# Kernel tuning notes

Measured on AMD Instinct MI355X. Metric: run time of the kernel, lower is better.

## Reference

```python
import jax, jax.numpy as jnp
import numpy as np
import math

EPS = 1e-5

def setup_inputs() -> dict:
    key = jax.random.key(0)
    ks = jax.random.split(key, 8)
    B, S, H, HD = 2, 4096, 2048, 128
    hidden_states = jax.random.normal(ks[0], (B, S, H), dtype=jnp.float32)
    attention_mask = jnp.zeros((1, S, S), dtype=jnp.float32)
    cos = jax.random.uniform(ks[1], (S, HD), dtype=jnp.float32)
    sin = jax.random.uniform(ks[2], (S, HD), dtype=jnp.float32)
    sc = 0.02
    wq = jax.random.normal(ks[3], (H, H), dtype=jnp.float32) * sc
    wk = jax.random.normal(ks[4], (H, H), dtype=jnp.float32) * sc
    wv = jax.random.normal(ks[5], (H, H), dtype=jnp.float32) * sc
    wo = jax.random.normal(ks[6], (H, H), dtype=jnp.float32) * sc
    return {"hidden_states": hidden_states, "attention_mask": attention_mask,
            "cos": cos, "sin": sin, "wq": wq, "wk": wk, "wv": wv, "wo": wo}


def _bitlinear(x, w):
    # BitNet 1.58b: ternarize weights (round(clamp(w/scale,-1,1))), dequant by mean|w|.
    scale = jnp.mean(jnp.abs(w))
    qw = jnp.round(jnp.clip(w / (scale + EPS), -1.0, 1.0))  # ternary {-1,0,1}
    dq = qw * scale
    return x @ dq.T


def _rotate_half(x):
    x1, x2 = jnp.split(x, 2, axis=-1)
    return jnp.concatenate((-x2, x1), axis=-1)


def _apply_rope(q, k, cos, sin):
    B, S, H = q.shape
    hd = cos.shape[-1]
    q4 = q.reshape(B, S, -1, hd)
    k4 = k.reshape(B, S, -1, hd)
    c = cos[None, :, None, :]  # [1,S,1,hd]
    s = sin[None, :, None, :]
    qe = q4 * c + _rotate_half(q4) * s
    ke = k4 * c + _rotate_half(k4) * s
    return qe.reshape(B, S, H), ke.reshape(B, S, H)


def reference(hidden_states, attention_mask, cos, sin, wq, wk, wv, wo):
    head_dim = cos.shape[-1]
    q = _bitlinear(hidden_states, wq)
    k = _bitlinear(hidden_states, wk)
    v = _bitlinear(hidden_states, wv)
    q, k = _apply_rope(q, k, cos, sin)
    # NOTE: original attends over the FULL hidden dim (no head split), scaled by sqrt(head_dim)
    scores = jnp.einsum('bqh,bkh->bqk', q, k) / math.sqrt(head_dim)
    scores = scores + attention_mask
    probs = jax.nn.softmax(scores, axis=-1)
    attn_out = jnp.einsum('bqk,bkh->bqh', probs, v)
    return _bitlinear(attn_out, wo)
```

## Files before the change

kernel.cpp:

```cpp
#include <hip/hip_runtime.h>
#include <hip/hip_bf16.h>
#include <stdint.h>

typedef _Float16 f16x8 __attribute__((ext_vector_type(8)));
typedef float f32x4 __attribute__((ext_vector_type(4)));
typedef unsigned short u16;

#define B_   2
#define S_   4096
#define H_   2048
#define M2_  8192
#define WELEMS (H_*H_)

__device__ __forceinline__ u16 f2h(float f) {
  _Float16 h = (_Float16)f;
  return __builtin_bit_cast(unsigned short, h);
}
__device__ __forceinline__ float h2f(u16 b) {
  _Float16 h = __builtin_bit_cast(_Float16, b);
  return (float)h;
}

__device__ __forceinline__ void gload16(const void* gptr, const void* lptr) {
  __builtin_amdgcn_global_load_lds(
      (const __attribute__((address_space(1))) void*)(uintptr_t)gptr,
      (__attribute__((address_space(3))) void*)(uint32_t)(uintptr_t)lptr,
      16, 0, 0);
}

template<int EPI>
__global__ __launch_bounds__(512, 2)
void gemm8(const u16* __restrict__ A, const u16* __restrict__ B,
           void* __restrict__ Cv, int K, int ldc, float cscale,
           long long sA, long long sB, long long sC)
{
  extern __shared__ char smem[];
  const int tid  = threadIdx.x;
  const int lane = tid & 63;
  const int wid  = tid >> 6;
  const int wm   = wid >> 2;
  const int wn   = wid & 3;

  const int gx  = gridDim.x;
  const int nwg = gx * gridDim.y;
  int f = blockIdx.y * gx + blockIdx.x;
  f = (f & 7) * (nwg >> 3) + (f >> 3);
  const int brow = (f / gx) << 8;
  const int bcol = (f % gx) << 8;
  const int z    = blockIdx.z;

  const u16* Ab = A + (size_t)z * sA;
  const u16* Bb = B + (size_t)z * sB;

  const int srow = ((tid >> 3) << 1) | ((tid >> 2) & 1);
  const int sk8  = (tid & 3) ^ ((tid >> 3) & 3);
  const u16* gA0 = Ab + (size_t)(brow + srow) * K + sk8 * 8;
  const u16* gA1 = gA0 + (size_t)128 * K;
  const u16* gB0 = Bb + (size_t)(bcol + srow) * K + sk8 * 8;
  const u16* gB1 = gB0 + (size_t)128 * K;

  char* ldsAw = smem + tid * 16;
  char* ldsBw = ldsAw + 65536;

  const int l15 = lane & 15;
  const int lanepart = ((l15 >> 1) << 7) |
                       ((((lane >> 4) ^ ((l15 >> 1) & 3))) << 4) |
                       ((lane & 1) << 6);
  const char* ldsA = smem + (wm << 13) + lanepart;
  const char* ldsB = smem + 65536 + (wn << 12) + lanepart;

  f32x4 acc[8][4];
  #pragma unroll
  for (int i = 0; i < 8; ++i)
    #pragma unroll
    for (int j = 0; j < 4; ++j) acc[i][j] = (f32x4){0.f, 0.f, 0.f, 0.f};

#define DS_A(BUF, MH, MR) (*(const f16x8*)(ldsA + (BUF)*16384 + (MH)*4096 + (MR)*1024))
#define DS_B(BUF, NR)     (*(const f16x8*)(ldsB + (BUF)*16384 + (NR)*1024))

#define MFMA4(AM, AV) \
  acc[AM][0] = __builtin_amdgcn_mfma_f32_16x16x32_f16(AV, b0, acc[AM][0], 0, 0, 0); \
  acc[AM][1] = __builtin_amdgcn_mfma_f32_16x16x32_f16(AV, b1, acc[AM][1], 0, 0, 0); \
  acc[AM][2] = __builtin_amdgcn_mfma_f32_16x16x32_f16(AV, b2, acc[AM][2], 0, 0, 0); \
  acc[AM][3] = __builtin_amdgcn_mfma_f32_16x16x32_f16(AV, b3, acc[AM][3], 0, 0, 0);

#define TILE(BUF, IBUF, DOISS, LASTT) do {                                    \
    if (LASTT) { asm volatile("s_waitcnt vmcnt(0)" ::: "memory"); }           \
    else       { asm volatile("s_waitcnt vmcnt(4)" ::: "memory"); }           \
    __builtin_amdgcn_s_barrier();                                             \
    if (DOISS) {                                                              \
      gload16(gA0, ldsAw + (IBUF)*16384);                                     \
      gload16(gA1, ldsAw + (IBUF)*16384 + 8192);                              \
    }                                                                         \
    f16x8 b0 = DS_B(BUF,0), b1 = DS_B(BUF,1), b2 = DS_B(BUF,2), b3 = DS_B(BUF,3); \
    f16x8 a0 = DS_A(BUF,0,0), a1 = DS_A(BUF,0,1), a2 = DS_A(BUF,0,2), a3 = DS_A(BUF,0,3); \
    asm volatile("s_waitcnt lgkmcnt(0)" ::: "memory");                        \
    __builtin_amdgcn_sched_barrier(0);                                        \
    __builtin_amdgcn_s_setprio(1);                                            \
    MFMA4(0, a0) MFMA4(1, a1) MFMA4(2, a2) MFMA4(3, a3)                       \
    __builtin_amdgcn_s_setprio(0);                                            \
    __builtin_amdgcn_s_barrier();                                             \
    if (DOISS) {                                                              \
      gload16(gB0, ldsBw + (IBUF)*16384);                                     \
      gload16(gB1, ldsBw + (IBUF)*16384 + 8192);                              \
      gA0 += 32; gA1 += 32; gB0 += 32; gB1 += 32;                             \
    }                                                                         \
    a0 = DS_A(BUF,1,0); a1 = DS_A(BUF,1,1); a2 = DS_A(BUF,1,2); a3 = DS_A(BUF,1,3); \
    asm volatile("s_waitcnt lgkmcnt(0)" ::: "memory");                        \
    __builtin_amdgcn_sched_barrier(0);                                        \
    __builtin_amdgcn_s_setprio(1);                                            \
    MFMA4(4, a0) MFMA4(5, a1) MFMA4(6, a2) MFMA4(7, a3)                       \
    __builtin_amdgcn_s_setprio(0);                                            \
  } while (0)

  gload16(gA0, ldsAw);          gload16(gA1, ldsAw + 8192);
  gload16(gB0, ldsBw);          gload16(gB1, ldsBw + 8192);
  gA0 += 32; gA1 += 32; gB0 += 32; gB1 += 32;
  gload16(gA0, ldsAw + 16384);  gload16(gA1, ldsAw + 16384 + 8192);
  gload16(gB0, ldsBw + 16384);  gload16(gB1, ldsBw + 16384 + 8192);
  gA0 += 32; gA1 += 32; gB0 += 32; gB1 += 32;

  const int NT4 = K >> 7;
  for (int it = 0; it < NT4; ++it) {
    const bool lst = (it == NT4 - 1);
    TILE(0, 2, true,  false);
    TILE(1, 3, true,  false);
    TILE(2, 0, !lst,  false);
    TILE(3, 1, !lst,  lst);
  }

#undef TILE
#undef MFMA4
#undef DS_A
#undef DS_B

  const float scv = cscale;
  const int cr0 = brow + (wm << 7) + ((lane >> 4) << 2);
  const int cc0 = bcol + (wn << 6) + l15;

  if constexpr (EPI == 0) {
    u16* C = (u16*)Cv + (size_t)z * sC;
    #pragma unroll
    for (int am = 0; am < 8; ++am) {
      const int r = cr0 + am * 16;
      #pragma unroll
      for (int an = 0; an < 4; ++an) {
        const int c = cc0 + an * 16;
        #pragma unroll
        for (int j = 0; j < 4; ++j)
          C[(size_t)(r + j) * ldc + c] = f2h(acc[am][an][j] * scv);
      }
    }
  } else if constexpr (EPI == 1) {
    u16* C = (u16*)Cv + (size_t)z * sC;
    #pragma unroll
    for (int am = 0; am < 8; ++am) {
      const int r = cr0 + am * 16;
      #pragma unroll
      for (int an = 0; an < 4; ++an) {
        const int c = cc0 + an * 16;
        ushort4 pk;
        pk.x = f2h(acc[am][an][0] * scv);
        pk.y = f2h(acc[am][an][1] * scv);
        pk.z = f2h(acc[am][an][2] * scv);
        pk.w = f2h(acc[am][an][3] * scv);
        *(ushort4*)&C[(size_t)c * ldc + r] = pk;
      }
    }
  } else {
    float* C = (float*)Cv + (size_t)z * sC;
    #pragma unroll
    for (int am = 0; am < 8; ++am) {
      const int r = cr0 + am * 16;
      #pragma unroll
      for (int an = 0; an < 4; ++an) {
        const int c = cc0 + an * 16;
        #pragma unroll
        for (int j = 0; j < 4; ++j)
          C[(size_t)(r + j) * ldc + c] = acc[am][an][j] * scv;
      }
    }
  }
}

__global__ __launch_bounds__(256)
void abssum_partial(const float* __restrict__ w0, const float* __restrict__ w1,
                    const float* __restrict__ w2, const float* __restrict__ w3,
                    float* __restrict__ part)
{
  const float* w = (blockIdx.y==0)?w0:(blockIdx.y==1)?w1:(blockIdx.y==2)?w2:w3;
  float s = 0.f;
  const int N4 = WELEMS/4;
  for (int i = blockIdx.x*256 + threadIdx.x; i < N4; i += 256*256) {
    float4 v = ((const float4*)w)[i];
    s += fabsf(v.x)+fabsf(v.y)+fabsf(v.z)+fabsf(v.w);
  }
  #pragma unroll
  for (int o=32;o;o>>=1) s += __shfl_xor(s,o);
  __shared__ float r[4];
  if ((threadIdx.x&63)==0) r[threadIdx.x>>6] = s;
  __syncthreads();
  if (threadIdx.x==0) part[blockIdx.y*256 + blockIdx.x] = (r[0]+r[1])+(r[2]+r[3]);
}

__global__ __launch_bounds__(256)
void scale_final(const float* __restrict__ part, float* __restrict__ scales)
{
  float s = part[blockIdx.x*256 + threadIdx.x];
  #pragma unroll
  for (int o=32;o;o>>=1) s += __shfl_xor(s,o);
  __shared__ float r[4];
  if ((threadIdx.x&63)==0) r[threadIdx.x>>6] = s;
  __syncthreads();
  if (threadIdx.x==0) scales[blockIdx.x] = ((r[0]+r[1])+(r[2]+r[3])) * (1.f/(float)WELEMS);
}

__global__ __launch_bounds__(256)
void dequant_w(const float* __restrict__ w0, const float* __restrict__ w1,
               const float* __restrict__ w2, const float* __restrict__ w3,
               const float* __restrict__ scales, u16* __restrict__ out)
{
  const int wi = blockIdx.y;
  const float* w = (wi==0)?w0:(wi==1)?w1:(wi==2)?w2:w3;
  u16* o = out + (size_t)wi * WELEMS;
  const float scv = scales[wi];
  const float inv = 1.f/(scv + 1e-5f);
  const int i0 = (blockIdx.x*256 + threadIdx.x)*8;
  float4 a = *(const float4*)(w + i0);
  float4 b = *(const float4*)(w + i0 + 4);
  float t[8] = {a.x,a.y,a.z,a.w,b.x,b.y,b.z,b.w};
  union { uint4 v; u16 h[8]; } r;
  #pragma unroll
  for (int j=0;j<8;++j){
    float x = t[j]*inv;
    x = fminf(fmaxf(x,-1.f),1.f);
    r.h[j] = f2h(rintf(x)*scv);
  }
  *(uint4*)(o + i0) = r.v;
}

__global__ __launch_bounds__(256)
void cast_f16(const float* __restrict__ x, u16* __restrict__ o)
{
  const int i0 = (blockIdx.x*256 + threadIdx.x)*8;
  float4 a = *(const float4*)(x + i0);
  float4 b = *(const float4*)(x + i0 + 4);
  float t[8] = {a.x,a.y,a.z,a.w,b.x,b.y,b.z,b.w};
  union { uint4 v; u16 h[8]; } r;
  #pragma unroll
  for (int j=0;j<8;++j) r.h[j] = f2h(t[j]);
  *(uint4*)(o + i0) = r.v;
}

__global__ __launch_bounds__(256)
void rope_qk(u16* __restrict__ Q, u16* __restrict__ K,
             const float* __restrict__ cosb, const float* __restrict__ sinb)
{
  const uint32_t idx = blockIdx.x*256 + threadIdx.x;
  const int d   = idx & 63;
  const int h16 = (idx >> 6) & 15;
  const int s   = (idx >> 10) & (S_-1);
  const int b   = idx >> 22;
  const size_t base = ((size_t)b*S_ + s)*H_ + h16*128 + d;
  const int ci = s*128 + d;
  const float c0 = cosb[ci], c1 = cosb[ci+64];
  const float s0 = sinb[ci], s1 = sinb[ci+64];
  const float q0 = h2f(Q[base]), q1 = h2f(Q[base+64]);
  Q[base]    = f2h(q0*c0 - q1*s0);
  Q[base+64] = f2h(q1*c1 + q0*s1);
  const float k0 = h2f(K[base]), k1 = h2f(K[base+64]);
  K[base]    = f2h(k0*c0 - k1*s0);
  K[base+64] = f2h(k1*c1 + k0*s1);
}

__global__ __launch_bounds__(256)
void softmax_h(u16* __restrict__ P, const float* __restrict__ mask)
{
  const int row = blockIdx.x;
  const int q   = row & (S_-1);
  u16* prow = P + (size_t)row * S_;
  const float* mrow = mask + (size_t)q * S_;
  const int tid  = threadIdx.x;
  const int lane = tid & 63;
  const int base = tid * 16;

  union { uint4 v[2]; u16 h[16]; } sv;
  sv.v[0] = *(const uint4*)(prow + base);
  sv.v[1] = *(const uint4*)(prow + base + 8);
  float mk[16];
  #pragma unroll
  for (int j=0;j<4;++j) ((float4*)mk)[j] = *(const float4*)(mrow + base + 4*j);

  float v[16];
  #pragma unroll
  for (int i=0;i<16;++i) v[i] = h2f(sv.h[i]) + mk[i];

  float mx = v[0];
  #pragma unroll
  for (int i=1;i<16;++i) mx = fmaxf(mx, v[i]);
  #pragma unroll
  for (int o=32;o;o>>=1) mx = fmaxf(mx, __shfl_xor(mx, o));
  __shared__ float red[8];
  if (lane==0) red[tid>>6] = mx;
  __syncthreads();
  mx = fmaxf(fmaxf(red[0],red[1]), fmaxf(red[2],red[3]));

  float e[16]; float sm = 0.f;
  #pragma unroll
  for (int i=0;i<16;++i){ e[i] = __expf(v[i]-mx); sm += e[i]; }
  #pragma unroll
  for (int o=32;o;o>>=1) sm += __shfl_xor(sm, o);
  if (lane==0) red[4 + (tid>>6)] = sm;
  __syncthreads();
  sm = (red[4]+red[5])+(red[6]+red[7]);
  const float inv = 1.f/sm;

  union { uint4 v[2]; u16 h[16]; } ov;
  #pragma unroll
  for (int i=0;i<16;++i) ov.h[i] = f2h(e[i]*inv);
  *(uint4*)(prow + base)     = ov.v[0];
  *(uint4*)(prow + base + 8) = ov.v[1];
}

__global__ void fill_f32(float* p, float v, int n) {
  int i = blockIdx.x*256 + threadIdx.x;
  if (i < n) p[i] = v;
}

extern "C" void kernel_launch(void* const* d_in, const int* in_sizes, int n_in,
                              void* d_out, int out_size, void* d_ws, size_t ws_size,
                              hipStream_t stream)
{
  const float* hs   = (const float*)d_in[0];
  const float* mask = (const float*)d_in[1];
  const float* cosb = (const float*)d_in[2];
  const float* sinb = (const float*)d_in[3];
  const float* wq   = (const float*)d_in[4];
  const float* wk   = (const float*)d_in[5];
  const float* wv   = (const float*)d_in[6];
  const float* wo   = (const float*)d_in[7];

  char* w = (char*)d_ws;
  const size_t SZ = (size_t)M2_ * H_ * 2;
  u16* Wh = (u16*)(w);
  u16* Xh = (u16*)(w + SZ);
  u16* Qh = (u16*)(w + 2*SZ);
  u16* Kh = (u16*)(w + 3*SZ);
  u16* AO = Qh;
  u16* Vt = Kh;
  float* part   = (float*)d_out;
  float* scales = part + 1024;
  u16* P  = (u16*)d_out;

  const size_t need = 4*SZ;
  if (ws_size < need || out_size != M2_*H_) {
    float v = (out_size != M2_*H_) ? 2.0e9f : (float)ws_size;
    fill_f32<<<dim3((out_size+255)/256), dim3(256), 0, stream>>>((float*)d_out, v, out_size);
    return;
  }

  dim3 blk(256), gblk(512);
  const size_t QOFF = (size_t)S_*H_;
  const float qksc = 0.08838834764831845f;

  abssum_partial<<<dim3(256,4), blk, 0, stream>>>(wq,wk,wv,wo, part);
  scale_final  <<<dim3(4),     blk, 0, stream>>>(part, scales);
  dequant_w    <<<dim3(WELEMS/(256*8),4), blk, 0, stream>>>(wq,wk,wv,wo, scales, Wh);
  cast_f16     <<<dim3((M2_*H_)/(256*8)), blk, 0, stream>>>(hs, Xh);

  gemm8<0><<<dim3(8,32,1), gblk, 131072, stream>>>(Xh, Wh,        Qh, H_, H_, 1.f, 0,0,0);
  gemm8<0><<<dim3(8,32,1), gblk, 131072, stream>>>(Xh, Wh+WELEMS, Kh, H_, H_, 1.f, 0,0,0);

  rope_qk<<<dim3((B_*S_*16*64)/256), blk, 0, stream>>>(Qh, Kh, cosb, sinb);

  gemm8<0><<<dim3(16,16,2), gblk, 131072, stream>>>(Qh, Kh, P, H_, S_, qksc,
      (long long)QOFF, (long long)QOFF, (long long)S_*S_);

  softmax_h<<<dim3(B_*S_), blk, 0, stream>>>(P, mask);

  gemm8<1><<<dim3(8,16,2), gblk, 131072, stream>>>(Xh, Wh+2*WELEMS, Vt, H_, S_, 1.f,
      (long long)QOFF, 0, (long long)H_*S_);

  gemm8<0><<<dim3(8,16,2), gblk, 131072, stream>>>(P, Vt, AO, S_, H_, 1.f,
      (long long)S_*S_, (long long)H_*S_, (long long)QOFF);

  gemm8<2><<<dim3(8,32,1), gblk, 131072, stream>>>(AO, Wh+3*WELEMS, d_out, H_, H_, 1.f, 0,0,0);
}
```

Baseline: 602.1 us.

## Double-buffer LDS fragment registers to overlap reads with MFMA in GEMM loop

Restructures the GEMM main loop so that the LDS fragments for the next k-tile are loaded into a second register set midway through the current tile's MFMA sequence. The two barriers per tile become a single barrier placed between the two MFMA halves, with explicit sched_barriers fixing the order. This is meant to hide LDS read latency and cut synchronisation stalls between MFMA bursts. In exchange it roughly doubles the fragment register footprint, which risks spills or lower occupancy.

```diff
diff --git a/kernel.cpp b/kernel.cpp
--- a/kernel.cpp
+++ b/kernel.cpp
@@ -75,42 +75,72 @@
     #pragma unroll
     for (int j = 0; j < 4; ++j) acc[i][j] = (f32x4){0.f, 0.f, 0.f, 0.f};
 
+  f16x8 A0_0{}, A0_1{}, A0_2{}, A0_3{}, A0_4{}, A0_5{}, A0_6{}, A0_7{};
+  f16x8 B0_0{}, B0_1{}, B0_2{}, B0_3{};
+  f16x8 A1_0{}, A1_1{}, A1_2{}, A1_3{}, A1_4{}, A1_5{}, A1_6{}, A1_7{};
+  f16x8 B1_0{}, B1_1{}, B1_2{}, B1_3{};
+
 #define DS_A(BUF, MH, MR) (*(const f16x8*)(ldsA + (BUF)*16384 + (MH)*4096 + (MR)*1024))
 #define DS_B(BUF, NR)     (*(const f16x8*)(ldsB + (BUF)*16384 + (NR)*1024))
 
-#define MFMA4(AM, AV) \
-  acc[AM][0] = __builtin_amdgcn_mfma_f32_16x16x32_f16(AV, b0, acc[AM][0], 0, 0, 0); \
-  acc[AM][1] = __builtin_amdgcn_mfma_f32_16x16x32_f16(AV, b1, acc[AM][1], 0, 0, 0); \
-  acc[AM][2] = __builtin_amdgcn_mfma_f32_16x16x32_f16(AV, b2, acc[AM][2], 0, 0, 0); \
-  acc[AM][3] = __builtin_amdgcn_mfma_f32_16x16x32_f16(AV, b3, acc[AM][3], 0, 0, 0);
-
-#define TILE(BUF, IBUF, DOISS, LASTT) do {                                    \
-    if (LASTT) { asm volatile("s_waitcnt vmcnt(0)" ::: "memory"); }           \
-    else       { asm volatile("s_waitcnt vmcnt(4)" ::: "memory"); }           \
-    __builtin_amdgcn_s_barrier();                                             \
+#define MF(av, bv, cc) __builtin_amdgcn_mfma_f32_16x16x32_f16(av, bv, cc, 0, 0, 0)
+
+#define CL0(S) \
+  acc[0][0]=MF(A##S##_0,B##S##_0,acc[0][0]); acc[0][1]=MF(A##S##_0,B##S##_1,acc[0][1]); \
+  acc[0][2]=MF(A##S##_0,B##S##_2,acc[0][2]); acc[0][3]=MF(A##S##_0,B##S##_3,acc[0][3]); \
+  acc[1][0]=MF(A##S##_1,B##S##_0,acc[1][0]); acc[1][1]=MF(A##S##_1,B##S##_1,acc[1][1]); \
+  acc[1][2]=MF(A##S##_1,B##S##_2,acc[1][2]); acc[1][3]=MF(A##S##_1,B##S##_3,acc[1][3]); \
+  acc[2][0]=MF(A##S##_2,B##S##_0,acc[2][0]); acc[2][1]=MF(A##S##_2,B##S##_1,acc[2][1]); \
+  acc[2][2]=MF(A##S##_2,B##S##_2,acc[2][2]); acc[2][3]=MF(A##S##_2,B##S##_3,acc[2][3]); \
+  acc[3][0]=MF(A##S##_3,B##S##_0,acc[3][0]); acc[3][1]=MF(A##S##_3,B##S##_1,acc[3][1]); \
+  acc[3][2]=MF(A##S##_3,B##S##_2,acc[3][2]); acc[3][3]=MF(A##S##_3,B##S##_3,acc[3][3]);
+
+#define CL1(S) \
+  acc[4][0]=MF(A##S##_4,B##S##_0,acc[4][0]); acc[4][1]=MF(A##S##_4,B##S##_1,acc[4][1]); \
+  acc[4][2]=MF(A##S##_4,B##S##_2,acc[4][2]); acc[4][3]=MF(A##S##_4,B##S##_3,acc[4][3]); \
+  acc[5][0]=MF(A##S##_5,B##S##_0,acc[5][0]); acc[5][1]=MF(A##S##_5,B##S##_1,acc[5][1]); \
+  acc[5][2]=MF(A##S##_5,B##S##_2,acc[5][2]); acc[5][3]=MF(A##S##_5,B##S##_3,acc[5][3]); \
+  acc[6][0]=MF(A##S##_6,B##S##_0,acc[6][0]); acc[6][1]=MF(A##S##_6,B##S##_1,acc[6][1]); \
+  acc[6][2]=MF(A##S##_6,B##S##_2,acc[6][2]); acc[6][3]=MF(A##S##_6,B##S##_3,acc[6][3]); \
+  acc[7][0]=MF(A##S##_7,B##S##_0,acc[7][0]); acc[7][1]=MF(A##S##_7,B##S##_1,acc[7][1]); \
+  acc[7][2]=MF(A##S##_7,B##S##_2,acc[7][2]); acc[7][3]=MF(A##S##_7,B##S##_3,acc[7][3]);
+
+#define READS(T, RBUF) \
+  B##T##_0 = DS_B(RBUF,0); B##T##_1 = DS_B(RBUF,1); \
+  B##T##_2 = DS_B(RBUF,2); B##T##_3 = DS_B(RBUF,3); \
+  A##T##_0 = DS_A(RBUF,0,0); A##T##_1 = DS_A(RBUF,0,1); \
+  A##T##_2 = DS_A(RBUF,0,2); A##T##_3 = DS_A(RBUF,0,3); \
+  A##T##_4 = DS_A(RBUF,1,0); A##T##_5 = DS_A(RBUF,1,1); \
+  A##T##_6 = DS_A(RBUF,1,2); A##T##_7 = DS_A(RBUF,1,3);
+
+#define TILE(BUF, RBUF, IBUF, S, T, DOISS, VMZ, EPIL) do {                    \
+    asm volatile("s_waitcnt lgkmcnt(0)" ::: "memory");                        \
+    __builtin_amdgcn_sched_barrier(0);                                        \
     if (DOISS) {                                                              \
       gload16(gA0, ldsAw + (IBUF)*16384);                                     \
       gload16(gA1, ldsAw + (IBUF)*16384 + 8192);                              \
-    }                                                                         \
-    f16x8 b0 = DS_B(BUF,0), b1 = DS_B(BUF,1), b2 = DS_B(BUF,2), b3 = DS_B(BUF,3); \
-    f16x8 a0 = DS_A(BUF,0,0), a1 = DS_A(BUF,0,1), a2 = DS_A(BUF,0,2), a3 = DS_A(BUF,0,3); \
-    asm volatile("s_waitcnt lgkmcnt(0)" ::: "memory");                        \
-    __builtin_amdgcn_sched_barrier(0);                                        \
-    __builtin_amdgcn_s_setprio(1);                                            \
-    MFMA4(0, a0) MFMA4(1, a1) MFMA4(2, a2) MFMA4(3, a3)                       \
-    __builtin_amdgcn_s_setprio(0);                                            \
-    __builtin_amdgcn_s_barrier();                                             \
-    if (DOISS) {                                                              \
       gload16(gB0, ldsBw + (IBUF)*16384);                                     \
       gload16(gB1, ldsBw + (IBUF)*16384 + 8192);                              \
       gA0 += 32; gA1 += 32; gB0 += 32; gB1 += 32;                             \
     }                                                                         \
-    a0 = DS_A(BUF,1,0); a1 = DS_A(BUF,1,1); a2 = DS_A(BUF,1,2); a3 = DS_A(BUF,1,3); \
-    asm volatile("s_waitcnt lgkmcnt(0)" ::: "memory");                        \
     __builtin_amdgcn_sched_barrier(0);                                        \
     __builtin_amdgcn_s_setprio(1);                                            \
-    MFMA4(4, a0) MFMA4(5, a1) MFMA4(6, a2) MFMA4(7, a3)                       \
+    CL0(S)                                                                    \
     __builtin_amdgcn_s_setprio(0);                                            \
+    __builtin_amdgcn_sched_barrier(0);                                        \
+    if (!(EPIL)) {                                                            \
+      if (VMZ) { asm volatile("s_waitcnt vmcnt(0)" ::: "memory"); }           \
+      else     { asm volatile("s_waitcnt vmcnt(4)" ::: "memory"); }           \
+      __builtin_amdgcn_sched_barrier(0);                                      \
+      __builtin_amdgcn_s_barrier();                                           \
+      __builtin_amdgcn_sched_barrier(0);                                      \
+      READS(T, RBUF)                                                          \
+      __builtin_amdgcn_sched_barrier(0);                                      \
+    }                                                                         \
+    __builtin_amdgcn_s_setprio(1);                                            \
+    CL1(S)                                                                    \
+    __builtin_amdgcn_s_setprio(0);                                            \
+    __builtin_amdgcn_sched_barrier(0);                                        \
   } while (0)
 
   gload16(gA0, ldsAw);          gload16(gA1, ldsAw + 8192);
@@ -119,18 +149,27 @@
   gload16(gA0, ldsAw + 16384);  gload16(gA1, ldsAw + 16384 + 8192);
   gload16(gB0, ldsBw + 16384);  gload16(gB1, ldsBw + 16384 + 8192);
   gA0 += 32; gA1 += 32; gB0 += 32; gB1 += 32;
+  asm volatile("s_waitcnt vmcnt(4)" ::: "memory");
+  __builtin_amdgcn_sched_barrier(0);
+  __builtin_amdgcn_s_barrier();
+  __builtin_amdgcn_sched_barrier(0);
+  READS(0, 0)
+  __builtin_amdgcn_sched_barrier(0);
 
   const int NT4 = K >> 7;
   for (int it = 0; it < NT4; ++it) {
     const bool lst = (it == NT4 - 1);
-    TILE(0, 2, true,  false);
-    TILE(1, 3, true,  false);
-    TILE(2, 0, !lst,  false);
-    TILE(3, 1, !lst,  lst);
+    TILE(0, 1, 2, 0, 1, true,  false, false);
+    TILE(1, 2, 3, 1, 0, true,  false, false);
+    TILE(2, 3, 0, 0, 1, !lst,  lst,   false);
+    TILE(3, 0, 1, 1, 0, !lst,  false, lst);
   }
 
 #undef TILE
-#undef MFMA4
+#undef READS
+#undef CL0
+#undef CL1
+#undef MF
 #undef DS_A
 #undef DS_B
 
```

After: 694.8 us. +15.4%, slower.

## Software-pipeline LDS fragment reads across K-tiles with one barrier per tile

Applied to the files above, without the earlier changes.

Restructures the GEMM main loop so the B and first A fragments of the next LDS tile are read while the current tile's MFMAs run. Two register sets alternate between tiles, and fine-grained lgkmcnt waits are interleaved between MFMA groups. The two barriers per tile become one, and all four global loads are issued together after the first half of the MFMAs. The aim is to hide LDS latency and cut synchronisation stalls, at the cost of more VGPRs (doubled fragment registers) and fragile hand-tuned waitcnt accounting.

```diff
diff --git a/kernel.cpp b/kernel.cpp
--- a/kernel.cpp
+++ b/kernel.cpp
@@ -75,42 +75,70 @@
     #pragma unroll
     for (int j = 0; j < 4; ++j) acc[i][j] = (f32x4){0.f, 0.f, 0.f, 0.f};
 
+  f16x8 FA0_0{}, FA0_1{}, FA0_2{}, FA0_3{}, FA0_4{}, FA0_5{}, FA0_6{}, FA0_7{};
+  f16x8 FB0_0{}, FB0_1{}, FB0_2{}, FB0_3{};
+  f16x8 FA1_0{}, FA1_1{}, FA1_2{}, FA1_3{}, FA1_4{}, FA1_5{}, FA1_6{}, FA1_7{};
+  f16x8 FB1_0{}, FB1_1{}, FB1_2{}, FB1_3{};
+
 #define DS_A(BUF, MH, MR) (*(const f16x8*)(ldsA + (BUF)*16384 + (MH)*4096 + (MR)*1024))
 #define DS_B(BUF, NR)     (*(const f16x8*)(ldsB + (BUF)*16384 + (NR)*1024))
 
-#define MFMA4(AM, AV) \
-  acc[AM][0] = __builtin_amdgcn_mfma_f32_16x16x32_f16(AV, b0, acc[AM][0], 0, 0, 0); \
-  acc[AM][1] = __builtin_amdgcn_mfma_f32_16x16x32_f16(AV, b1, acc[AM][1], 0, 0, 0); \
-  acc[AM][2] = __builtin_amdgcn_mfma_f32_16x16x32_f16(AV, b2, acc[AM][2], 0, 0, 0); \
-  acc[AM][3] = __builtin_amdgcn_mfma_f32_16x16x32_f16(AV, b3, acc[AM][3], 0, 0, 0);
-
-#define TILE(BUF, IBUF, DOISS, LASTT) do {                                    \
-    if (LASTT) { asm volatile("s_waitcnt vmcnt(0)" ::: "memory"); }           \
-    else       { asm volatile("s_waitcnt vmcnt(4)" ::: "memory"); }           \
-    __builtin_amdgcn_s_barrier();                                             \
+#define MF(av, bv, cc) __builtin_amdgcn_mfma_f32_16x16x32_f16(av, bv, cc, 0, 0, 0)
+
+#define CLROW(S, M) \
+  acc[M][0]=MF(FA##S##_##M, FB##S##_0, acc[M][0]); \
+  acc[M][1]=MF(FA##S##_##M, FB##S##_1, acc[M][1]); \
+  acc[M][2]=MF(FA##S##_##M, FB##S##_2, acc[M][2]); \
+  acc[M][3]=MF(FA##S##_##M, FB##S##_3, acc[M][3]);
+
+#define RD_A27(S, BUF) \
+  FA##S##_2 = DS_A(BUF,0,2); FA##S##_3 = DS_A(BUF,0,3); \
+  FA##S##_4 = DS_A(BUF,1,0); FA##S##_5 = DS_A(BUF,1,1); \
+  FA##S##_6 = DS_A(BUF,1,2); FA##S##_7 = DS_A(BUF,1,3);
+
+#define RD_BA01(S, BUF) \
+  FB##S##_0 = DS_B(BUF,0); FB##S##_1 = DS_B(BUF,1); \
+  FB##S##_2 = DS_B(BUF,2); FB##S##_3 = DS_B(BUF,3); \
+  FA##S##_0 = DS_A(BUF,0,0); FA##S##_1 = DS_A(BUF,0,1);
+
+#define SBAR __builtin_amdgcn_sched_barrier(0)
+
+#define TILE(CUR, NXT, GLD, S, T, DOISS, DORD) do {                           \
+    asm volatile("s_waitcnt lgkmcnt(0)" ::: "memory");     \
+    SBAR;                                                                     \
+    RD_A27(S, CUR)                           \
+    SBAR;                                                                     \
+    __builtin_amdgcn_s_setprio(1); CLROW(S,0) CLROW(S,1)                      \
+    __builtin_amdgcn_s_setprio(0); SBAR;                                      \
+    asm volatile("s_waitcnt lgkmcnt(4)" ::: "memory");       \
+    SBAR;                                                                     \
+    __builtin_amdgcn_s_setprio(1); CLROW(S,2) CLROW(S,3)                      \
+    __builtin_amdgcn_s_setprio(0); SBAR;                                      \
     if (DOISS) {                                                              \
-      gload16(gA0, ldsAw + (IBUF)*16384);                                     \
-      gload16(gA1, ldsAw + (IBUF)*16384 + 8192);                              \
+      gload16(gA0, ldsAw + (GLD)*16384);                                      \
+      gload16(gA1, ldsAw + (GLD)*16384 + 8192);                               \
+      gload16(gB0, ldsBw + (GLD)*16384);                                      \
+      gload16(gB1, ldsBw + (GLD)*16384 + 8192);                               \
+      gA0 += 32; gA1 += 32; gB0 += 32; gB1 += 32;                             \
+      asm volatile("s_waitcnt vmcnt(4)" ::: "memory");    \
+    } else {                                                                  \
+      asm volatile("s_waitcnt vmcnt(0)" ::: "memory");                        \
     }                                                                         \
-    f16x8 b0 = DS_B(BUF,0), b1 = DS_B(BUF,1), b2 = DS_B(BUF,2), b3 = DS_B(BUF,3); \
-    f16x8 a0 = DS_A(BUF,0,0), a1 = DS_A(BUF,0,1), a2 = DS_A(BUF,0,2), a3 = DS_A(BUF,0,3); \
-    asm volatile("s_waitcnt lgkmcnt(0)" ::: "memory");                        \
-    __builtin_amdgcn_sched_barrier(0);                                        \
-    __builtin_amdgcn_s_setprio(1);                                            \
-    MFMA4(0, a0) MFMA4(1, a1) MFMA4(2, a2) MFMA4(3, a3)                       \
-    __builtin_amdgcn_s_setprio(0);                                            \
-    __builtin_amdgcn_s_barrier();                                             \
-    if (DOISS) {                                                              \
-      gload16(gB0, ldsBw + (IBUF)*16384);                                     \
-      gload16(gB1, ldsBw + (IBUF)*16384 + 8192);                              \
-      gA0 += 32; gA1 += 32; gB0 += 32; gB1 += 32;                             \
-    }                                                                         \
-    a0 = DS_A(BUF,1,0); a1 = DS_A(BUF,1,1); a2 = DS_A(BUF,1,2); a3 = DS_A(BUF,1,3); \
-    asm volatile("s_waitcnt lgkmcnt(0)" ::: "memory");                        \
-    __builtin_amdgcn_sched_barrier(0);                                        \
-    __builtin_amdgcn_s_setprio(1);                                            \
-    MFMA4(4, a0) MFMA4(5, a1) MFMA4(6, a2) MFMA4(7, a3)                       \
-    __builtin_amdgcn_s_setprio(0);                                            \
+    SBAR;                                                                     \
+    __builtin_amdgcn_s_barrier();            \
+    SBAR;                                                                     \
+    if (DORD) { RD_BA01(T, NXT) }                  \
+    SBAR;                                                                     \
+    if (DORD) { asm volatile("s_waitcnt lgkmcnt(8)" ::: "memory"); }          \
+    else      { asm volatile("s_waitcnt lgkmcnt(2)" ::: "memory"); }          \
+    SBAR;                                                    \
+    __builtin_amdgcn_s_setprio(1); CLROW(S,4) CLROW(S,5)                      \
+    __builtin_amdgcn_s_setprio(0); SBAR;                                      \
+    if (DORD) { asm volatile("s_waitcnt lgkmcnt(6)" ::: "memory"); }          \
+    else      { asm volatile("s_waitcnt lgkmcnt(0)" ::: "memory"); }          \
+    SBAR;                                                    \
+    __builtin_amdgcn_s_setprio(1); CLROW(S,6) CLROW(S,7)                      \
+    __builtin_amdgcn_s_setprio(0); SBAR;                                      \
   } while (0)
 
   gload16(gA0, ldsAw);          gload16(gA1, ldsAw + 8192);
@@ -119,20 +147,33 @@
   gload16(gA0, ldsAw + 16384);  gload16(gA1, ldsAw + 16384 + 8192);
   gload16(gB0, ldsBw + 16384);  gload16(gB1, ldsBw + 16384 + 8192);
   gA0 += 32; gA1 += 32; gB0 += 32; gB1 += 32;
+  asm volatile("s_waitcnt vmcnt(4)" ::: "memory");
+  SBAR;
+  __builtin_amdgcn_s_barrier();
+  SBAR;
+  RD_BA01(0, 0)
+  SBAR;
 
   const int NT4 = K >> 7;
-  for (int it = 0; it < NT4; ++it) {
-    const bool lst = (it == NT4 - 1);
-    TILE(0, 2, true,  false);
-    TILE(1, 3, true,  false);
-    TILE(2, 0, !lst,  false);
-    TILE(3, 1, !lst,  lst);
+  for (int it = 0; it < NT4 - 1; ++it) {
+    TILE(0, 1, 2, 0, 1, true, true);
+    TILE(1, 2, 3, 1, 0, true, true);
+    TILE(2, 3, 0, 0, 1, true, true);
+    TILE(3, 0, 1, 1, 0, true, true);
   }
+  TILE(0, 1, 2, 0, 1, true,  true);
+  TILE(1, 2, 3, 1, 0, true,  true);
+  TILE(2, 3, 0, 0, 1, false, true);
+  TILE(3, 0, 1, 1, 0, false, false);
 
 #undef TILE
-#undef MFMA4
+#undef RD_BA01
+#undef RD_A27
+#undef CLROW
+#undef MF
 #undef DS_A
 #undef DS_B
+#undef SBAR
 
   const float scv = cscale;
   const int cr0 = brow + (wm << 7) + ((lane >> 4) << 2);
```

Measured after the change: 599.9 us. About the same (-0.4%).
